# Optimization experiments

Measured on AMD Instinct MI355X. Metric: run time of the kernel, lower is better.

## Reference

```python
import jax, jax.numpy as jnp
import numpy as np


def _hilbert_filter(S):
    # scipy.signal.hilbert analytic-signal spectrum multiplier
    h = np.zeros(S, dtype=np.float32)
    h[0] = 1.0
    if S % 2 == 0:
        h[S // 2] = 1.0
        h[1:S // 2] = 2.0
    else:
        h[1:(S + 1) // 2] = 2.0
    return h


def setup_inputs() -> dict:
    key = jax.random.key(0)
    B, C, S = 16, 64, 2048
    x = jax.random.normal(key, (B, C, S), dtype=jnp.float32)
    return {"x": x}


def reference(x) -> jnp.ndarray:
    B, C, S = x.shape
    h = jnp.asarray(_hilbert_filter(S))
    # Analytic signal via FFT (batched over all B*C channels at once,
    # instead of recomputing hilbert() per (i,j) pair as the torch loop does)
    analytic = jnp.fft.ifft(jnp.fft.fft(x, axis=-1) * h, axis=-1)  # [B,C,S] complex
    theta = jnp.angle(analytic)                                    # [B,C,S]
    # Pairwise instantaneous phase differences: [B,C,C,S]
    d = theta[:, :, None, :] - theta[:, None, :, :]
    # angle(exp(1j*d)) wraps d to (-pi,pi]; original zeroes exact +/-pi values.
    # sign(sin(d)) == sign(wrapped d) with +/-pi (and 0) mapped to 0 -- identical math.
    pli = jnp.abs(jnp.mean(jnp.sign(jnp.sin(d)), axis=-1))         # [B,C,C]
    # diagonal: d == 0 -> sign 0 -> mean 0, matching the skipped i==j entries
    return pli.astype(jnp.float32)
```

## Files before the change

### kernel.cpp

```cpp
#include <hip/hip_runtime.h>

#define Bv 16
#define Cv 64
#define Sv 2048
#define NSEG 64
#define SSEG 32
#define ROWS 68
#define NTILE 144

__device__ __forceinline__ void bf_f(float2& u, float2& v, const float2 w) {
    const float dr = u.x - v.x, di = u.y - v.y;
    u.x += v.x; u.y += v.y;
    v.x = dr * w.x - di * w.y;
    v.y = dr * w.y + di * w.x;
}
__device__ __forceinline__ void bf_i(float2& u, float2& v, const float2 w) {
    const float vr = v.x * w.x + v.y * w.y;
    const float vi = v.y * w.x - v.x * w.y;
    v.x = u.x - vr; v.y = u.y - vi;
    u.x += vr; u.y += vi;
}
__device__ __forceinline__ float2 csq(const float2 a) {
    return make_float2(a.x * a.x - a.y * a.y, 2.0f * a.x * a.y);
}
__device__ __forceinline__ float2 cm1(const float2 a) {
    const float cq = 0.70710678118654752f;
    return make_float2(cq * (a.x + a.y), cq * (a.y - a.x));
}
__device__ __forceinline__ float2 cmi(const float2 a) {
    return make_float2(a.y, -a.x);
}
__device__ __forceinline__ int pad(int n) { return n + (n >> 3); }

__global__ __launch_bounds__(256) void hilbert_kernel(const float* __restrict__ x,
                                                      float* __restrict__ y) {
    __shared__ float2 zz[Sv + Sv / 8];
    const int t = threadIdx.x;
    const int c0 = blockIdx.x * 2;
    const float* x0 = x + (size_t)c0 * Sv;
    const float* x1 = x0 + Sv;

    const float PI = 3.14159265358979323846f;
    float2 bA4, bB4, bC2;
    sincosf(-PI * (float)t * (1.0f / 1024.0f), &bA4.y, &bA4.x);
    sincosf(-PI * (float)(t & 31) * (1.0f / 128.0f), &bB4.y, &bB4.x);
    sincosf(-PI * (float)(t & 7) * (1.0f / 16.0f), &bC2.y, &bC2.x);
    const float2 bA2 = csq(bA4), bA1 = csq(bA2);
    const float2 bB2 = csq(bB4), bB1 = csq(bB2);
    const float2 bC1 = csq(bC2);

    float2 z[8];
    #pragma unroll
    for (int k = 0; k < 8; ++k)
        z[k] = make_float2(x0[t + 256 * k], x1[t + 256 * k]);

    {
        const float2 w1 = cm1(bA4);
        bf_f(z[0], z[4], bA4);      bf_f(z[1], z[5], w1);
        bf_f(z[2], z[6], cmi(bA4)); bf_f(z[3], z[7], cmi(w1));
        const float2 wB = cmi(bA2);
        bf_f(z[0], z[2], bA2); bf_f(z[1], z[3], wB);
        bf_f(z[4], z[6], bA2); bf_f(z[5], z[7], wB);
        bf_f(z[0], z[1], bA1); bf_f(z[2], z[3], bA1);
        bf_f(z[4], z[5], bA1); bf_f(z[6], z[7], bA1);
    }
    #pragma unroll
    for (int k = 0; k < 8; ++k) zz[pad(t + 256 * k)] = z[k];
    __syncthreads();

    {
        const int r = t & 31, base = (t >> 5) * 256 + r;
        #pragma unroll
        for (int k = 0; k < 8; ++k) z[k] = zz[pad(base + 32 * k)];
        const float2 w1 = cm1(bB4);
        bf_f(z[0], z[4], bB4);      bf_f(z[1], z[5], w1);
        bf_f(z[2], z[6], cmi(bB4)); bf_f(z[3], z[7], cmi(w1));
        const float2 wB = cmi(bB2);
        bf_f(z[0], z[2], bB2); bf_f(z[1], z[3], wB);
        bf_f(z[4], z[6], bB2); bf_f(z[5], z[7], wB);
        bf_f(z[0], z[1], bB1); bf_f(z[2], z[3], bB1);
        bf_f(z[4], z[5], bB1); bf_f(z[6], z[7], bB1);
        #pragma unroll
        for (int k = 0; k < 8; ++k) zz[pad(base + 32 * k)] = z[k];
    }
    __syncthreads();

    {
        const int r = t & 7, base0 = (t >> 3) * 32 + r, base1 = base0 + 1024;
        #pragma unroll
        for (int k = 0; k < 4; ++k) {
            z[k] = zz[pad(base0 + 8 * k)];
            z[4 + k] = zz[pad(base1 + 8 * k)];
        }
        const float2 wB = cmi(bC2);
        bf_f(z[0], z[2], bC2); bf_f(z[1], z[3], wB);
        bf_f(z[4], z[6], bC2); bf_f(z[5], z[7], wB);
        bf_f(z[0], z[1], bC1); bf_f(z[2], z[3], bC1);
        bf_f(z[4], z[5], bC1); bf_f(z[6], z[7], bC1);
        #pragma unroll
        for (int k = 0; k < 4; ++k) {
            zz[pad(base0 + 8 * k)] = z[k];
            zz[pad(base1 + 8 * k)] = z[4 + k];
        }
    }
    __syncthreads();

    {
        const int base = 8 * t;
        #pragma unroll
        for (int k = 0; k < 8; ++k) z[k] = zz[pad(base + k)];
        const float cq = 0.70710678118654752f;
        const float2 W1  = make_float2(1.0f, 0.0f);
        const float2 W41 = make_float2(cq, -cq);
        const float2 W42 = make_float2(0.0f, -1.0f);
        const float2 W43 = make_float2(-cq, -cq);
        bf_f(z[0], z[4], W1);  bf_f(z[1], z[5], W41);
        bf_f(z[2], z[6], W42); bf_f(z[3], z[7], W43);
        bf_f(z[0], z[2], W1); bf_f(z[1], z[3], W42);
        bf_f(z[4], z[6], W1); bf_f(z[5], z[7], W42);
        bf_f(z[0], z[1], W1); bf_f(z[2], z[3], W1);
        bf_f(z[4], z[5], W1); bf_f(z[6], z[7], W1);
        const float inv = 1.0f / (float)Sv;
        #pragma unroll
        for (int k = 0; k < 8; ++k) {
            const int kk = (int)(__brev((unsigned)(base + k)) >> 21);
            const float m = (kk == 0 || kk == Sv / 2) ? inv : (kk < Sv / 2 ? 2.0f * inv : 0.0f);
            z[k].x *= m; z[k].y *= m;
        }
        bf_i(z[0], z[1], W1); bf_i(z[2], z[3], W1);
        bf_i(z[4], z[5], W1); bf_i(z[6], z[7], W1);
        bf_i(z[0], z[2], W1); bf_i(z[1], z[3], W42);
        bf_i(z[4], z[6], W1); bf_i(z[5], z[7], W42);
        bf_i(z[0], z[4], W1);  bf_i(z[1], z[5], W41);
        bf_i(z[2], z[6], W42); bf_i(z[3], z[7], W43);
        #pragma unroll
        for (int k = 0; k < 8; ++k) zz[pad(base + k)] = z[k];
    }
    __syncthreads();

    {
        const int r = t & 7, base0 = (t >> 3) * 32 + r, base1 = base0 + 1024;
        #pragma unroll
        for (int k = 0; k < 4; ++k) {
            z[k] = zz[pad(base0 + 8 * k)];
            z[4 + k] = zz[pad(base1 + 8 * k)];
        }
        bf_i(z[0], z[1], bC1); bf_i(z[2], z[3], bC1);
        bf_i(z[4], z[5], bC1); bf_i(z[6], z[7], bC1);
        const float2 wB = cmi(bC2);
        bf_i(z[0], z[2], bC2); bf_i(z[1], z[3], wB);
        bf_i(z[4], z[6], bC2); bf_i(z[5], z[7], wB);
        #pragma unroll
        for (int k = 0; k < 4; ++k) {
            zz[pad(base0 + 8 * k)] = z[k];
            zz[pad(base1 + 8 * k)] = z[4 + k];
        }
    }
    __syncthreads();

    {
        const int r = t & 31, base = (t >> 5) * 256 + r;
        #pragma unroll
        for (int k = 0; k < 8; ++k) z[k] = zz[pad(base + 32 * k)];
        bf_i(z[0], z[1], bB1); bf_i(z[2], z[3], bB1);
        bf_i(z[4], z[5], bB1); bf_i(z[6], z[7], bB1);
        const float2 wB = cmi(bB2);
        bf_i(z[0], z[2], bB2); bf_i(z[1], z[3], wB);
        bf_i(z[4], z[6], bB2); bf_i(z[5], z[7], wB);
        const float2 w1 = cm1(bB4);
        bf_i(z[0], z[4], bB4);      bf_i(z[1], z[5], w1);
        bf_i(z[2], z[6], cmi(bB4)); bf_i(z[3], z[7], cmi(w1));
        #pragma unroll
        for (int k = 0; k < 8; ++k) zz[pad(base + 32 * k)] = z[k];
    }
    __syncthreads();

    {
        #pragma unroll
        for (int k = 0; k < 8; ++k) z[k] = zz[pad(t + 256 * k)];
        bf_i(z[0], z[1], bA1); bf_i(z[2], z[3], bA1);
        bf_i(z[4], z[5], bA1); bf_i(z[6], z[7], bA1);
        const float2 wB = cmi(bA2);
        bf_i(z[0], z[2], bA2); bf_i(z[1], z[3], wB);
        bf_i(z[4], z[6], bA2); bf_i(z[5], z[7], wB);
        const float2 w1 = cm1(bA4);
        bf_i(z[0], z[4], bA4);      bf_i(z[1], z[5], w1);
        bf_i(z[2], z[6], cmi(bA4)); bf_i(z[3], z[7], cmi(w1));
        float* y0 = y + (size_t)c0 * Sv;
        float* y1 = y0 + Sv;
        #pragma unroll
        for (int k = 0; k < 8; ++k) {
            const int n = t + 256 * k;
            y0[n] = z[k].y - x1[n];
            y1[n] = x0[n] - z[k].x;
        }
    }
}

__global__ __launch_bounds__(256) void pli_count_kernel(const float* __restrict__ x,
                                                        const float* __restrict__ y,
                                                        unsigned int* __restrict__ part) {
    __shared__ __align__(16) float xL[SSEG * ROWS];
    __shared__ __align__(16) float yL[SSEG * ROWS];
    const int blk = blockIdx.x;
    const int seg = blk & (NSEG - 1);
    const int b = blk >> 6;
    const int t = threadIdx.x;
    const float* xb = x + (size_t)b * Cv * Sv + seg * SSEG;
    const float* yb = y + (size_t)b * Cv * Sv + seg * SSEG;

    for (int e = t; e < Cv * SSEG; e += 256) {
        const int ch = e >> 5;
        const int s = e & (SSEG - 1);
        xL[s * ROWS + ch] = xb[(size_t)ch * Sv + s];
        yL[s * ROWS + ch] = yb[(size_t)ch * Sv + s];
    }
    __syncthreads();

    if (t < NTILE) {
        const int qi = t & 15;
        const int dq = t >> 4;
        const int i0 = qi * 4;
        const int j0 = ((qi + dq) & 15) * 4;
        int neg[4][4] = {};

        #pragma unroll 4
        for (int s = 0; s < SSEG; ++s) {
            const float4 xi = *(const float4*)&xL[s * ROWS + i0];
            const float4 yi = *(const float4*)&yL[s * ROWS + i0];
            const float4 xj = *(const float4*)&xL[s * ROWS + j0];
            const float4 yj = *(const float4*)&yL[s * ROWS + j0];
            const float xia[4] = {xi.x, xi.y, xi.z, xi.w};
            const float yia[4] = {yi.x, yi.y, yi.z, yi.w};
            const float xja[4] = {xj.x, xj.y, xj.z, xj.w};
            const float yja[4] = {yj.x, yj.y, yj.z, yj.w};
            #pragma unroll
            for (int a = 0; a < 4; ++a) {
                #pragma unroll
                for (int c = 0; c < 4; ++c) {
                    const float cr = fmaf(yia[a], xja[c], -(xia[a] * yja[c]));
                    neg[a][c] += (int)(__float_as_uint(cr) >> 31);
                }
            }
        }

        unsigned int* Pb = part + ((size_t)blk * NTILE + t) * 4;
        unsigned int pk[4];
        #pragma unroll
        for (int a = 0; a < 4; ++a)
            pk[a] = (unsigned)neg[a][0] | ((unsigned)neg[a][1] << 8)
                  | ((unsigned)neg[a][2] << 16) | ((unsigned)neg[a][3] << 24);
        *(uint4*)Pb = make_uint4(pk[0], pk[1], pk[2], pk[3]);
    }
}

__global__ __launch_bounds__(256) void finalize_kernel(const unsigned char* __restrict__ part,
                                                       float* __restrict__ out) {
    const int idx = blockIdx.x * 256 + threadIdx.x;
    const int b = idx >> 12;
    const int ij = idx & 4095;
    const int i = ij >> 6, j = ij & 63;
    const int qi = i >> 2, a = i & 3;
    const int qj = j >> 2, c = j & 3;
    const int g = (qj - qi) & 15;
    int byteoff;
    if (g <= 8) byteoff = (g * 16 + qi) * 16 + a * 4 + c;
    else        byteoff = ((16 - g) * 16 + qj) * 16 + c * 4 + a;
    const unsigned char* p = part + (size_t)b * NSEG * (NTILE * 16) + byteoff;
    int negsum = 0;
    #pragma unroll 8
    for (int s = 0; s < NSEG; ++s)
        negsum += (int)p[s * (NTILE * 16)];
    out[idx] = (i == j) ? 0.0f
                        : fabsf((float)Sv - 2.0f * (float)negsum) * (1.0f / (float)Sv);
}

extern "C" void kernel_launch(void* const* d_in, const int* in_sizes, int n_in,
                              void* d_out, int out_size, void* d_ws, size_t ws_size,
                              hipStream_t stream) {
    const float* x = (const float*)d_in[0];
    float* y = (float*)d_ws;
    unsigned int* part = (unsigned int*)((char*)d_ws + (size_t)Bv * Cv * Sv * sizeof(float));
    float* out = (float*)d_out;

    hipLaunchKernelGGL(hilbert_kernel, dim3(Bv * Cv / 2), dim3(256), 0, stream, x, y);
    hipLaunchKernelGGL(pli_count_kernel, dim3(Bv * NSEG), dim3(256), 0, stream, x, y, part);
    hipLaunchKernelGGL(finalize_kernel, dim3(Bv * Cv * Cv / 256), dim3(256), 0, stream,
                       (const unsigned char*)part, out);
}
```

Baseline: 82.45 us.

## Quantize phase to 32-bit fixed point and compare by wrapped integer subtraction

The Hilbert kernel now computes each sample's phase with atan2f and stores it as a fixed-point unsigned integer scaled so that 2*pi maps to 2^32. The pairwise count kernel then takes the sign of the wrapped phase difference from the top bit of a modular integer subtraction, replacing the float cross-product. This halves the shared-memory and global traffic in the count kernel and cuts its inner loop to one integer subtract and shift per pair. In exchange it adds atan2 work to the Hilbert kernel and risks rare sign differences near zero or pi caused by quantization.

```diff
diff --git a/kernel.cpp b/kernel.cpp
--- a/kernel.cpp
+++ b/kernel.cpp
@@ -33,7 +33,7 @@
 __device__ __forceinline__ int pad(int n) { return n + (n >> 3); }
 
 __global__ __launch_bounds__(256) void hilbert_kernel(const float* __restrict__ x,
-                                                      float* __restrict__ y) {
+                                                      unsigned int* __restrict__ u) {
     __shared__ float2 zz[Sv + Sv / 8];
     const int t = threadIdx.x;
     const int c0 = blockIdx.x * 2;
@@ -186,34 +186,34 @@
         const float2 w1 = cm1(bA4);
         bf_i(z[0], z[4], bA4);      bf_i(z[1], z[5], w1);
         bf_i(z[2], z[6], cmi(bA4)); bf_i(z[3], z[7], cmi(w1));
-        float* y0 = y + (size_t)c0 * Sv;
-        float* y1 = y0 + Sv;
+        unsigned int* u0 = u + (size_t)c0 * Sv;
+        unsigned int* u1 = u0 + Sv;
+        const float SC = 683565275.576f;
         #pragma unroll
         for (int k = 0; k < 8; ++k) {
             const int n = t + 256 * k;
-            y0[n] = z[k].y - x1[n];
-            y1[n] = x0[n] - z[k].x;
-        }
-    }
-}
-
-__global__ __launch_bounds__(256) void pli_count_kernel(const float* __restrict__ x,
-                                                        const float* __restrict__ y,
+            const float xa = x0[n], xb = x1[n];
+            const float ha = z[k].y - xb;
+            const float hb = xa - z[k].x;
+            u0[n] = (unsigned int)__float2int_rz(atan2f(ha, xa) * SC);
+            u1[n] = (unsigned int)__float2int_rz(atan2f(hb, xb) * SC);
+        }
+    }
+}
+
+__global__ __launch_bounds__(256) void pli_count_kernel(const unsigned int* __restrict__ u,
                                                         unsigned int* __restrict__ part) {
-    __shared__ __align__(16) float xL[SSEG * ROWS];
-    __shared__ __align__(16) float yL[SSEG * ROWS];
+    __shared__ __align__(16) unsigned int uL[SSEG * ROWS];
     const int blk = blockIdx.x;
     const int seg = blk & (NSEG - 1);
     const int b = blk >> 6;
     const int t = threadIdx.x;
-    const float* xb = x + (size_t)b * Cv * Sv + seg * SSEG;
-    const float* yb = y + (size_t)b * Cv * Sv + seg * SSEG;
+    const unsigned int* ub = u + (size_t)b * Cv * Sv + seg * SSEG;
 
     for (int e = t; e < Cv * SSEG; e += 256) {
         const int ch = e >> 5;
         const int s = e & (SSEG - 1);
-        xL[s * ROWS + ch] = xb[(size_t)ch * Sv + s];
-        yL[s * ROWS + ch] = yb[(size_t)ch * Sv + s];
+        uL[s * ROWS + ch] = ub[(size_t)ch * Sv + s];
     }
     __syncthreads();
 
@@ -226,20 +226,15 @@
 
         #pragma unroll 4
         for (int s = 0; s < SSEG; ++s) {
-            const float4 xi = *(const float4*)&xL[s * ROWS + i0];
-            const float4 yi = *(const float4*)&yL[s * ROWS + i0];
-            const float4 xj = *(const float4*)&xL[s * ROWS + j0];
-            const float4 yj = *(const float4*)&yL[s * ROWS + j0];
-            const float xia[4] = {xi.x, xi.y, xi.z, xi.w};
-            const float yia[4] = {yi.x, yi.y, yi.z, yi.w};
-            const float xja[4] = {xj.x, xj.y, xj.z, xj.w};
-            const float yja[4] = {yj.x, yj.y, yj.z, yj.w};
+            const uint4 ui = *(const uint4*)&uL[s * ROWS + i0];
+            const uint4 uj = *(const uint4*)&uL[s * ROWS + j0];
+            const unsigned int uia[4] = {ui.x, ui.y, ui.z, ui.w};
+            const unsigned int uja[4] = {uj.x, uj.y, uj.z, uj.w};
             #pragma unroll
             for (int a = 0; a < 4; ++a) {
                 #pragma unroll
                 for (int c = 0; c < 4; ++c) {
-                    const float cr = fmaf(yia[a], xja[c], -(xia[a] * yja[c]));
-                    neg[a][c] += (int)(__float_as_uint(cr) >> 31);
+                    neg[a][c] += (int)((uia[a] - uja[c]) >> 31);
                 }
             }
         }
@@ -279,12 +274,12 @@
                               void* d_out, int out_size, void* d_ws, size_t ws_size,
                               hipStream_t stream) {
     const float* x = (const float*)d_in[0];
-    float* y = (float*)d_ws;
-    unsigned int* part = (unsigned int*)((char*)d_ws + (size_t)Bv * Cv * Sv * sizeof(float));
+    unsigned int* u = (unsigned int*)d_ws;
+    unsigned int* part = (unsigned int*)((char*)d_ws + (size_t)Bv * Cv * Sv * sizeof(unsigned int));
     float* out = (float*)d_out;
 
-    hipLaunchKernelGGL(hilbert_kernel, dim3(Bv * Cv / 2), dim3(256), 0, stream, x, y);
-    hipLaunchKernelGGL(pli_count_kernel, dim3(Bv * NSEG), dim3(256), 0, stream, x, y, part);
+    hipLaunchKernelGGL(hilbert_kernel, dim3(Bv * Cv / 2), dim3(256), 0, stream, x, u);
+    hipLaunchKernelGGL(pli_count_kernel, dim3(Bv * NSEG), dim3(256), 0, stream, u, part);
     hipLaunchKernelGGL(finalize_kernel, dim3(Bv * Cv * Cv / 256), dim3(256), 0, stream,
                        (const unsigned char*)part, out);
 }
```

Result: no change. 81.66 us (-1.0%).
